# Kernel optimization log

Hardware: AMD Instinct MI355X
Metric: run time of the kernel (lower is better)

Reference implementation:

```python
import jax, jax.numpy as jnp
import numpy as np

WINDOW = 5
PAD = 2  # (window_size - 1) // 2 for dilation=1


def _layernorm(x, gamma, beta, eps=1e-5):
    # fp32 LayerNorm over last dim, cast back to input dtype
    orig = x.dtype
    x32 = x.astype(jnp.float32)
    mu = jnp.mean(x32, axis=-1, keepdims=True)
    var = jnp.var(x32, axis=-1, keepdims=True)
    y = (x32 - mu) * jax.lax.rsqrt(var + eps) * gamma + beta
    return y.astype(orig)


def _forward(x, ln_gamma, ln_beta, T):
    L, N, D = x.shape  # L = 1 + P tokens, N = B*T
    P = L - 1
    B = N // T
    xn = _layernorm(x, ln_gamma, ln_beta)

    # UnfoldTemporalWindows: x[1:] -> (N, D, P) -> (B, T, D, P), window over T
    patches = jnp.transpose(xn[1:], (1, 2, 0))            # (N, D, P)
    xv = patches.reshape(B, T, D, P)
    xp = jnp.pad(xv, ((0, 0), (PAD, PAD), (0, 0), (0, 0)))
    idx = jnp.arange(T)[:, None] + jnp.arange(WINDOW)[None, :]  # (T, W)
    win = xp[:, idx]                                       # (B, T, W, D, P)
    win = jnp.transpose(win, (0, 1, 3, 2, 4)).reshape(N, D, WINDOW * P)
    upfold = jnp.transpose(win, (2, 0, 1))                 # (O, N, D), O = W*P

    # Correlation_Module: sigmoid affinity of CLS token vs windowed tokens
    cls = xn[:1]                                           # (1, N, D)
    aff = jnp.einsum('lnd,ond->lon', cls, upfold) / jnp.sqrt(jnp.asarray(D, cls.dtype))
    feat = jnp.einsum('lon,ond->lnd', jax.nn.sigmoid(aff) - 0.5, upfold)
    return feat  # (1, N, D)


def setup_inputs() -> dict:
    key = jax.random.key(0)
    k1, = jax.random.split(key, 1)
    L, N, D = 197, 128, 768
    x = jax.random.normal(k1, (L, N, D), dtype=jnp.float32)
    ln_gamma = jnp.ones((D,), dtype=jnp.float32)
    ln_beta = jnp.zeros((D,), dtype=jnp.float32)
    return {"x": x, "ln_gamma": ln_gamma, "ln_beta": ln_beta, "T": 16}


def reference(x, ln_gamma, ln_beta, T):
    return _forward(x, ln_gamma, ln_beta, T)
```

## Files before the change

kernel.cpp:

```cpp
#include <hip/hip_runtime.h>

#define NN 128
#define DD 768
#define TT 16
#define PP 196
#define NSL 98
#define SCL 0.03608439182435161f

typedef short short8 __attribute__((ext_vector_type(8)));
typedef short short4v __attribute__((ext_vector_type(4)));
typedef float f32x4 __attribute__((ext_vector_type(4)));

static __device__ __forceinline__ ushort f2bf(float f) {
    union { float f; unsigned int u; } a; a.f = f;
    unsigned int r = a.u + 0x7fffu + ((a.u >> 16) & 1u);
    return (ushort)(r >> 16);
}
static __device__ __forceinline__ float bf2f(ushort u) {
    union { unsigned int u; float f; } c; c.u = (unsigned int)u << 16; return c.f;
}

static __device__ __forceinline__ int vidx(int r, int d) {
    return r * DD + ((((d >> 3) ^ (r & 7)) << 3) | (d & 7));
}

static __device__ __forceinline__ void bar_lgkm() {
    asm volatile("s_waitcnt lgkmcnt(0)" ::: "memory");
    __builtin_amdgcn_s_barrier();
    __builtin_amdgcn_sched_barrier(0);
}

__global__ __launch_bounds__(256) void k_lnq(const float* __restrict__ x,
                                             const float* __restrict__ gamma,
                                             const float* __restrict__ beta,
                                             ushort* __restrict__ qn,
                                             float* __restrict__ out) {
    int zi = blockIdx.x * 256 + threadIdx.x;
    float4 z = {0.f, 0.f, 0.f, 0.f};
    ((float4*)out)[zi]         = z;
    ((float4*)out)[zi + 8192]  = z;
    ((float4*)out)[zi + 16384] = z;

    int row  = (blockIdx.x << 2) + (threadIdx.x >> 6);
    int lane = threadIdx.x & 63;
    const float4* xr = (const float4*)(x + (size_t)row * DD);
    float4 v[3];
    float s = 0.f, ss = 0.f;
#pragma unroll
    for (int j = 0; j < 3; ++j) {
        v[j] = xr[lane + 64 * j];
        s  += v[j].x + v[j].y + v[j].z + v[j].w;
        ss = fmaf(v[j].x, v[j].x, ss); ss = fmaf(v[j].y, v[j].y, ss);
        ss = fmaf(v[j].z, v[j].z, ss); ss = fmaf(v[j].w, v[j].w, ss);
    }
#pragma unroll
    for (int o = 32; o > 0; o >>= 1) { s += __shfl_xor(s, o); ss += __shfl_xor(ss, o); }
    float mu  = s * (1.f / DD);
    float var = fmaf(ss, 1.f / DD, -mu * mu);
    float rs  = rsqrtf(var + 1e-5f);
    const float4* g4 = (const float4*)gamma;
    const float4* b4 = (const float4*)beta;
    ushort4* outr = (ushort4*)(qn + (size_t)row * DD);
#pragma unroll
    for (int j = 0; j < 3; ++j) {
        int i4 = lane + 64 * j;
        float4 g = g4[i4], b = b4[i4];
        ushort4 o4;
        o4.x = f2bf((v[j].x - mu) * rs * g.x + b.x);
        o4.y = f2bf((v[j].y - mu) * rs * g.y + b.y);
        o4.z = f2bf((v[j].z - mu) * rs * g.z + b.z);
        o4.w = f2bf((v[j].w - mu) * rs * g.w + b.w);
        outr[i4] = o4;
    }
}

template<bool USE_PART>
__global__ __launch_bounds__(512, 4) void k_attn(const float* __restrict__ x,
                                                 const float* __restrict__ gamma,
                                                 const float* __restrict__ beta,
                                                 const ushort* __restrict__ qn,
                                                 ushort* __restrict__ part,
                                                 float* __restrict__ out) {
    __shared__ ushort Vl[32 * DD];
    __shared__ float  Sl[8][TT][33];
    __shared__ ushort Wl[TT][32];

    int gid = blockIdx.x;
    int b = gid & 7, sl = gid >> 3;
    int w = threadIdx.x >> 6, l = threadIdx.x & 63;
    int l15 = l & 15, lh = l >> 4;

    {
        int r = threadIdx.x >> 4, j = threadIdx.x & 15;
        const float* vrow =
            x + ((size_t)(1 + sl * 2 + (r >> 4)) * NN + b * TT + (r & 15)) * DD;
        float4 c[12];
#pragma unroll
        for (int k = 0; k < 12; ++k) c[k] = *(const float4*)(vrow + (j + 16 * k) * 4);
        float s1 = 0.f, s2 = 0.f;
#pragma unroll
        for (int k = 0; k < 12; ++k) {
            float4 v = c[k];
            s1 += v.x + v.y + v.z + v.w;
            s2 = fmaf(v.x, v.x, s2); s2 = fmaf(v.y, v.y, s2);
            s2 = fmaf(v.z, v.z, s2); s2 = fmaf(v.w, v.w, s2);
        }
#pragma unroll
        for (int o = 1; o < 16; o <<= 1) { s1 += __shfl_xor(s1, o); s2 += __shfl_xor(s2, o); }
        float mu  = s1 * (1.f / DD);
        float var = fmaf(s2, 1.f / DD, -mu * mu);
        float rs  = rsqrtf(var + 1e-5f);
        const float4* g4 = (const float4*)gamma;
        const float4* b4 = (const float4*)beta;
#pragma unroll
        for (int k = 0; k < 12; ++k) {
            int c4 = j + 16 * k;
            float4 g = g4[c4], e = b4[c4];
            float4 v = c[k];
            ushort4 ut;
            ut.x = f2bf((v.x - mu) * rs * g.x + e.x);
            ut.y = f2bf((v.y - mu) * rs * g.y + e.y);
            ut.z = f2bf((v.z - mu) * rs * g.z + e.z);
            ut.w = f2bf((v.w - mu) * rs * g.w + e.w);
            *(ushort4*)&Vl[vidx(r, c4 * 4)] = ut;
        }
    }
    bar_lgkm();

    {
        const ushort* qrow = qn + (size_t)(b * TT + l15) * DD + w * 96 + lh * 8;
        short8 qf[3];
#pragma unroll
        for (int s = 0; s < 3; ++s) qf[s] = *(const short8*)(qrow + s * 32);
#pragma unroll
        for (int cg = 0; cg < 2; ++cg) {
            f32x4 sacc = (f32x4){0.f, 0.f, 0.f, 0.f};
            int vr = cg * 16 + l15;
#pragma unroll
            for (int s = 0; s < 3; ++s) {
                int k0 = w * 96 + s * 32 + lh * 8;
                short8 bfr = *(const short8*)&Vl[vidx(vr, k0)];
                sacc = __builtin_amdgcn_mfma_f32_16x16x32_bf16(qf[s], bfr, sacc, 0, 0, 0);
            }
#pragma unroll
            for (int q = 0; q < 4; ++q) Sl[w][lh * 4 + q][cg * 16 + l15] = sacc[q];
        }
    }
    bar_lgkm();

    {
        int t  = threadIdx.x >> 5, rr = threadIdx.x & 31;
        float s = 0.f;
#pragma unroll
        for (int k = 0; k < 8; ++k) s += Sl[k][t][rr];
        int m = rr & 15;
        int dlt = m - t;
        float wv = (dlt <= 2 && dlt >= -2)
                     ? (1.f / (1.f + __expf(-s * SCL)) - 0.5f) : 0.f;
        Wl[t][rr] = f2bf(wv);
    }
    bar_lgkm();

    f32x4 acc[6];
    {
        short8 wfrag = *(const short8*)&Wl[l15][lh * 8];
#pragma unroll
        for (int i = 0; i < 6; ++i) {
            int d0 = w * 96 + i * 16;
            union { ushort sv[8]; short8 v; } u;
#pragma unroll
            for (int j = 0; j < 8; ++j)
                u.sv[j] = Vl[vidx(lh * 8 + j, d0 + l15)];
            acc[i] = __builtin_amdgcn_mfma_f32_16x16x32_bf16(
                wfrag, u.v, (f32x4){0.f, 0.f, 0.f, 0.f}, 0, 0, 0);
        }
    }

    if (USE_PART) {
        ushort* myp = part + (size_t)(sl * 8 + b) * (TT * DD);
#pragma unroll
        for (int i = 0; i < 6; ++i) {
            ushort4 pk;
            pk.x = f2bf(acc[i][0]); pk.y = f2bf(acc[i][1]);
            pk.z = f2bf(acc[i][2]); pk.w = f2bf(acc[i][3]);
            *(ushort4*)&myp[((w * 6 + i) * 64 + l) * 4] = pk;
        }
    } else {
#pragma unroll
        for (int i = 0; i < 6; ++i) {
            int d0 = w * 96 + i * 16;
#pragma unroll
            for (int q = 0; q < 4; ++q)
                atomicAdd(out + (size_t)(b * TT + lh * 4 + q) * DD + d0 + l15, acc[i][q]);
        }
    }
}

__global__ __launch_bounds__(256) void k_reduce(const ushort* __restrict__ part,
                                                float* __restrict__ out) {
    int bid = blockIdx.x;
    int pc  = bid % 7;
    int g   = (bid / 7) * 256 + threadIdx.x;
    int b    = g / 3072;
    int pos4 = g - b * 3072;
    const ushort* src = part + (size_t)b * (TT * DD) + pos4 * 4;

    float s0 = 0.f, s1 = 0.f, s2 = 0.f, s3 = 0.f;
#pragma unroll 2
    for (int s = pc * 14; s < pc * 14 + 14; ++s) {
        union { short4v v; ushort sv[4]; } u;
        u.v = *(const short4v*)(src + (size_t)s * 8 * (TT * DD));
        s0 += bf2f(u.sv[0]); s1 += bf2f(u.sv[1]);
        s2 += bf2f(u.sv[2]); s3 += bf2f(u.sv[3]);
    }
    int fp    = pos4 * 4;
    int chunk = fp >> 8;
    int l     = (fp >> 2) & 63;
    int w     = chunk / 6, i = chunk - w * 6;
    int lh    = l >> 4,   l15 = l & 15;
    int d     = w * 96 + i * 16 + l15;
    float* dst = out + ((size_t)b * TT + lh * 4) * DD + d;
    atomicAdd(dst,          s0);
    atomicAdd(dst + 1 * DD, s1);
    atomicAdd(dst + 2 * DD, s2);
    atomicAdd(dst + 3 * DD, s3);
}

extern "C" void kernel_launch(void* const* d_in, const int* in_sizes, int n_in,
                              void* d_out, int out_size, void* d_ws, size_t ws_size,
                              hipStream_t stream) {
    const float* x     = (const float*)d_in[0];
    const float* gamma = (const float*)d_in[1];
    const float* beta  = (const float*)d_in[2];
    float* out = (float*)d_out;

    const size_t qn_bytes   = (size_t)NN * DD * 2;
    const size_t part_bytes = (size_t)NSL * 8 * TT * DD * 2;
    ushort* qn   = (ushort*)d_ws;
    ushort* part = (ushort*)((char*)d_ws + qn_bytes);
    bool use_part = ws_size >= qn_bytes + part_bytes;

    k_lnq<<<NN / 4, 256, 0, stream>>>(x, gamma, beta, qn, out);
    if (use_part) {
        k_attn<true><<<8 * NSL, 512, 0, stream>>>(x, gamma, beta, qn, part, out);
        k_reduce<<<7 * 96, 256, 0, stream>>>(part, out);
    } else {
        k_attn<false><<<8 * NSL, 512, 0, stream>>>(x, gamma, beta, qn, part, out);
    }
}
```

Baseline: 38.67 us.

## Fuse CLS LayerNorm into attention kernel and replace zeroing with memset

Removes the separate LayerNorm-of-query kernel. Each attention block now normalizes the 16 CLS rows for its batch itself, stages them through shared memory and loads the MFMA query fragments from there. Output zeroing moves to hipMemsetAsync, and the launch-bounds occupancy hint of 4 is dropped. This saves a kernel launch and the qn workspace round trip, but every one of the 784 blocks now recomputes the same CLS LayerNorm, which adds redundant global reads and an extra barrier phase.

```diff
diff --git a/kernel.cpp b/kernel.cpp
--- a/kernel.cpp
+++ b/kernel.cpp
@@ -30,57 +30,12 @@
     __builtin_amdgcn_sched_barrier(0);
 }
 
-__global__ __launch_bounds__(256) void k_lnq(const float* __restrict__ x,
-                                             const float* __restrict__ gamma,
-                                             const float* __restrict__ beta,
-                                             ushort* __restrict__ qn,
-                                             float* __restrict__ out) {
-    int zi = blockIdx.x * 256 + threadIdx.x;
-    float4 z = {0.f, 0.f, 0.f, 0.f};
-    ((float4*)out)[zi]         = z;
-    ((float4*)out)[zi + 8192]  = z;
-    ((float4*)out)[zi + 16384] = z;
-
-    int row  = (blockIdx.x << 2) + (threadIdx.x >> 6);
-    int lane = threadIdx.x & 63;
-    const float4* xr = (const float4*)(x + (size_t)row * DD);
-    float4 v[3];
-    float s = 0.f, ss = 0.f;
-#pragma unroll
-    for (int j = 0; j < 3; ++j) {
-        v[j] = xr[lane + 64 * j];
-        s  += v[j].x + v[j].y + v[j].z + v[j].w;
-        ss = fmaf(v[j].x, v[j].x, ss); ss = fmaf(v[j].y, v[j].y, ss);
-        ss = fmaf(v[j].z, v[j].z, ss); ss = fmaf(v[j].w, v[j].w, ss);
-    }
-#pragma unroll
-    for (int o = 32; o > 0; o >>= 1) { s += __shfl_xor(s, o); ss += __shfl_xor(ss, o); }
-    float mu  = s * (1.f / DD);
-    float var = fmaf(ss, 1.f / DD, -mu * mu);
-    float rs  = rsqrtf(var + 1e-5f);
-    const float4* g4 = (const float4*)gamma;
-    const float4* b4 = (const float4*)beta;
-    ushort4* outr = (ushort4*)(qn + (size_t)row * DD);
-#pragma unroll
-    for (int j = 0; j < 3; ++j) {
-        int i4 = lane + 64 * j;
-        float4 g = g4[i4], b = b4[i4];
-        ushort4 o4;
-        o4.x = f2bf((v[j].x - mu) * rs * g.x + b.x);
-        o4.y = f2bf((v[j].y - mu) * rs * g.y + b.y);
-        o4.z = f2bf((v[j].z - mu) * rs * g.z + b.z);
-        o4.w = f2bf((v[j].w - mu) * rs * g.w + b.w);
-        outr[i4] = o4;
-    }
-}
-
 template<bool USE_PART>
-__global__ __launch_bounds__(512, 4) void k_attn(const float* __restrict__ x,
-                                                 const float* __restrict__ gamma,
-                                                 const float* __restrict__ beta,
-                                                 const ushort* __restrict__ qn,
-                                                 ushort* __restrict__ part,
-                                                 float* __restrict__ out) {
+__global__ __launch_bounds__(512) void k_attn(const float* __restrict__ x,
+                                              const float* __restrict__ gamma,
+                                              const float* __restrict__ beta,
+                                              ushort* __restrict__ part,
+                                              float* __restrict__ out) {
     __shared__ ushort Vl[32 * DD];
     __shared__ float  Sl[8][TT][33];
     __shared__ ushort Wl[TT][32];
@@ -89,6 +44,66 @@
     int b = gid & 7, sl = gid >> 3;
     int w = threadIdx.x >> 6, l = threadIdx.x & 63;
     int l15 = l & 15, lh = l >> 4;
+
+    const float4* g4 = (const float4*)gamma;
+    const float4* b4 = (const float4*)beta;
+
+    {
+        const float* qra = x + (size_t)(b * TT + 2 * w) * DD;
+        const float* qrb = x + (size_t)(b * TT + 2 * w + 1) * DD;
+        float4 qa[3], qb[3];
+#pragma unroll
+        for (int k = 0; k < 3; ++k) {
+            qa[k] = ((const float4*)qra)[l + 64 * k];
+            qb[k] = ((const float4*)qrb)[l + 64 * k];
+        }
+        float a1 = 0.f, a2 = 0.f, c1 = 0.f, c2 = 0.f;
+#pragma unroll
+        for (int k = 0; k < 3; ++k) {
+            float4 v = qa[k];
+            a1 += v.x + v.y + v.z + v.w;
+            a2 = fmaf(v.x, v.x, a2); a2 = fmaf(v.y, v.y, a2);
+            a2 = fmaf(v.z, v.z, a2); a2 = fmaf(v.w, v.w, a2);
+            float4 u = qb[k];
+            c1 += u.x + u.y + u.z + u.w;
+            c2 = fmaf(u.x, u.x, c2); c2 = fmaf(u.y, u.y, c2);
+            c2 = fmaf(u.z, u.z, c2); c2 = fmaf(u.w, u.w, c2);
+        }
+#pragma unroll
+        for (int o = 32; o > 0; o >>= 1) {
+            a1 += __shfl_xor(a1, o); a2 += __shfl_xor(a2, o);
+            c1 += __shfl_xor(c1, o); c2 += __shfl_xor(c2, o);
+        }
+        float mua = a1 * (1.f / DD), mub = c1 * (1.f / DD);
+        float rsa = rsqrtf(fmaf(a2, 1.f / DD, -mua * mua) + 1e-5f);
+        float rsb = rsqrtf(fmaf(c2, 1.f / DD, -mub * mub) + 1e-5f);
+#pragma unroll
+        for (int k = 0; k < 3; ++k) {
+            int i4 = l + 64 * k;
+            float4 g = g4[i4], e = b4[i4];
+            float4 v = qa[k];
+            ushort4 ua;
+            ua.x = f2bf((v.x - mua) * rsa * g.x + e.x);
+            ua.y = f2bf((v.y - mua) * rsa * g.y + e.y);
+            ua.z = f2bf((v.z - mua) * rsa * g.z + e.z);
+            ua.w = f2bf((v.w - mua) * rsa * g.w + e.w);
+            *(ushort4*)&Vl[vidx(2 * w, i4 * 4)] = ua;
+            float4 u = qb[k];
+            ushort4 ub;
+            ub.x = f2bf((u.x - mub) * rsb * g.x + e.x);
+            ub.y = f2bf((u.y - mub) * rsb * g.y + e.y);
+            ub.z = f2bf((u.z - mub) * rsb * g.z + e.z);
+            ub.w = f2bf((u.w - mub) * rsb * g.w + e.w);
+            *(ushort4*)&Vl[vidx(2 * w + 1, i4 * 4)] = ub;
+        }
+    }
+    bar_lgkm();
+
+    short8 qf[3];
+#pragma unroll
+    for (int s = 0; s < 3; ++s)
+        qf[s] = *(const short8*)&Vl[vidx(l15, w * 96 + s * 32 + lh * 8)];
+    bar_lgkm();
 
     {
         int r = threadIdx.x >> 4, j = threadIdx.x & 15;
@@ -110,8 +125,6 @@
         float mu  = s1 * (1.f / DD);
         float var = fmaf(s2, 1.f / DD, -mu * mu);
         float rs  = rsqrtf(var + 1e-5f);
-        const float4* g4 = (const float4*)gamma;
-        const float4* b4 = (const float4*)beta;
 #pragma unroll
         for (int k = 0; k < 12; ++k) {
             int c4 = j + 16 * k;
@@ -128,10 +141,6 @@
     bar_lgkm();
 
     {
-        const ushort* qrow = qn + (size_t)(b * TT + l15) * DD + w * 96 + lh * 8;
-        short8 qf[3];
-#pragma unroll
-        for (int s = 0; s < 3; ++s) qf[s] = *(const short8*)(qrow + s * 32);
 #pragma unroll
         for (int cg = 0; cg < 2; ++cg) {
             f32x4 sacc = (f32x4){0.f, 0.f, 0.f, 0.f};
@@ -234,17 +243,15 @@
     const float* beta  = (const float*)d_in[2];
     float* out = (float*)d_out;
 
-    const size_t qn_bytes   = (size_t)NN * DD * 2;
     const size_t part_bytes = (size_t)NSL * 8 * TT * DD * 2;
-    ushort* qn   = (ushort*)d_ws;
-    ushort* part = (ushort*)((char*)d_ws + qn_bytes);
-    bool use_part = ws_size >= qn_bytes + part_bytes;
-
-    k_lnq<<<NN / 4, 256, 0, stream>>>(x, gamma, beta, qn, out);
+    ushort* part = (ushort*)d_ws;
+    bool use_part = ws_size >= part_bytes;
+
+    hipMemsetAsync(d_out, 0, (size_t)NN * DD * sizeof(float), stream);
     if (use_part) {
-        k_attn<true><<<8 * NSL, 512, 0, stream>>>(x, gamma, beta, qn, part, out);
+        k_attn<true><<<8 * NSL, 512, 0, stream>>>(x, gamma, beta, part, out);
         k_reduce<<<7 * 96, 256, 0, stream>>>(part, out);
     } else {
-        k_attn<false><<<8 * NSL, 512, 0, stream>>>(x, gamma, beta, qn, part, out);
-    }
-}
+        k_attn<false><<<8 * NSL, 512, 0, stream>>>(x, gamma, beta, part, out);
+    }
+}
```

After: 49.28 us. +27.4%, slower.
